# Kernel optimization log

Hardware: AMD Instinct MI355X
Metric: run time of the kernel (lower is better)

## Reference

```python
import jax, jax.numpy as jnp
import numpy as np

START_TAG = 1
END_TAG = 2
NUM_TAGS = 16


def setup_inputs() -> dict:
    key = jax.random.key(0)
    k1, k2, k3 = jax.random.split(key, 3)
    bs, L, T = 4096, 512, NUM_TAGS
    emission = jax.random.normal(k1, (bs, L, T), dtype=jnp.float32)
    tags = jax.random.randint(k2, (bs, L), 0, T, dtype=jnp.int64)
    mask = jnp.ones((bs, L), dtype=jnp.float32)
    # learned transition parameter, initialized as in the torch module
    transition = jax.random.uniform(k3, (T, T), minval=-0.1, maxval=0.1, dtype=jnp.float32)
    transition = transition.at[:, START_TAG].set(-1000.0)
    transition = transition.at[END_TAG, :].set(-1000.0)
    return {"emission": emission, "tags": tags, "mask": mask, "transition": transition}


def _compute_score(emission, tags, mask, transition):
    bs, L, T = emission.shape
    first = tags[:, 0]
    score = transition[START_TAG, first] + jnp.take_along_axis(
        emission[:, 0, :], first[:, None], axis=1).squeeze(1)
    prev_t = tags[:, :-1]
    cur_t = tags[:, 1:]
    trans_s = transition[prev_t, cur_t] * mask[:, 1:]
    em_s = jnp.take_along_axis(emission[:, 1:, :], cur_t[:, :, None], axis=2).squeeze(-1) * mask[:, 1:]
    score = score + (trans_s + em_s).sum(axis=1)
    last_idx = mask.astype(jnp.int32).sum(axis=1) - 1
    last_tags = jnp.take_along_axis(tags, last_idx[:, None].astype(tags.dtype), axis=1).squeeze(1)
    return score + transition[last_tags, END_TAG]


def _compute_dp(emission, mask, transition):
    bs, L, T = emission.shape

    def step(alpha, xs):
        em_t, m_t = xs  # em_t: [bs, T], m_t: [bs]
        # temp[b, prev, cur] = alpha[b, prev] + transition[prev, cur] + em_t[b, cur]
        new = jax.nn.logsumexp(
            alpha[:, :, None] + transition[None, :, :] + em_t[:, None, :], axis=1)
        alpha = m_t[:, None] * new + (1.0 - m_t[:, None]) * alpha
        return alpha, None

    alpha0 = jnp.zeros((bs, T), dtype=emission.dtype)  # faithful: torch.full(.., 0)
    alpha, _ = jax.lax.scan(step, alpha0, (jnp.swapaxes(emission, 0, 1), mask.T))
    alpha = alpha + transition[:, END_TAG][None, :]
    return jax.nn.logsumexp(alpha, axis=1)


def reference(emission, tags, mask, transition):
    score = _compute_score(emission, tags, mask, transition)
    dp = _compute_dp(emission, mask, transition)
    return -jnp.sum(score - dp)
```

## Files before the change

kernel.cpp:

```cpp
#include <hip/hip_runtime.h>

#define BS 4096
#define LL 512
#define NB 16
#define NCH 32
#define HT 256
#define SCWD 130
#define SCW 260
#define START_TAG 1
#define END_TAG 2
#define BIASF 4.5f
#define L2E 1.44269504f
#define LN2 0.69314718055994531f

typedef float f32x4 __attribute__((ext_vector_type(4)));
typedef short s16x4 __attribute__((ext_vector_type(4)));
union BF4 { unsigned u[2]; s16x4 s; };

__device__ __forceinline__ unsigned cvt_pk_bf16(float lo, float hi) {
    unsigned r;
    asm("v_cvt_pk_bf16_f32 %0, %1, %2" : "=v"(r) : "v"(lo), "v"(hi));
    return r;
}
__device__ __forceinline__ float blo(unsigned u) { return __uint_as_float(u << 16); }
__device__ __forceinline__ float bhi(unsigned u) { return __uint_as_float(u & 0xFFFF0000u); }
__device__ __forceinline__ float b2f(unsigned short h) { return __uint_as_float(((unsigned)h) << 16); }

__device__ __forceinline__ void chain16(const unsigned* __restrict__ sSC, int t0l,
                                        int j, int q, const BF4& Af, unsigned mb,
                                        unsigned& p01, unsigned& p23, float& e2f)
{
    const int base = t0l * SCWD + j * 8 + 2 * q;
    uint2 svA = *(const uint2*)(sSC + base);
    if (__all(mb == 0xFFFFu)) {
#pragma unroll
        for (int s = 0; s < 16; ++s) {
            const uint2 svB = (s < 15) ? *(const uint2*)(sSC + base + (s + 1) * SCWD) : svA;
            const float f0 = blo(svA.x), f1 = bhi(svA.x);
            const float f2 = blo(svA.y), f3 = bhi(svA.y);
            BF4 Bf; Bf.u[0] = p01; Bf.u[1] = p23;
            f32x4 z = {0.f, 0.f, 0.f, 0.f};
            f32x4 d = __builtin_amdgcn_mfma_f32_16x16x16bf16_1k(Af.s, Bf.s, z, 0, 0, 0);
            p01 = cvt_pk_bf16(d[0] * f0, d[1] * f1);
            p23 = cvt_pk_bf16(d[2] * f2, d[3] * f3);
            svA = svB;
        }
    } else {
#pragma unroll
        for (int s = 0; s < 16; ++s) {
            const uint2 svB = (s < 15) ? *(const uint2*)(sSC + base + (s + 1) * SCWD) : svA;
            const float f0 = blo(svA.x), f1 = bhi(svA.x);
            const float f2 = blo(svA.y), f3 = bhi(svA.y);
            BF4 Bf; Bf.u[0] = p01; Bf.u[1] = p23;
            f32x4 z = {0.f, 0.f, 0.f, 0.f};
            f32x4 d = __builtin_amdgcn_mfma_f32_16x16x16bf16_1k(Af.s, Bf.s, z, 0, 0, 0);
            const unsigned n01 = cvt_pk_bf16(d[0] * f0, d[1] * f1);
            const unsigned n23 = cvt_pk_bf16(d[2] * f2, d[3] * f3);
            const bool up = ((mb >> s) & 1u) != 0u;
            p01 = up ? n01 : p01;
            p23 = up ? n23 : p23;
            svA = svB;
        }
    }
    const float v0 = blo(p01), v1 = bhi(p01), v2 = blo(p23), v3 = bhi(p23);
    float mm = fmaxf(fmaxf(v0, v1), fmaxf(v2, v3));
    mm = fmaxf(mm, __shfl_xor(mm, 16));
    mm = fmaxf(mm, __shfl_xor(mm, 32));
    if (mm > 0.f) {
        const int ex = (int)((__float_as_uint(mm) >> 23) & 0xFFu) - 127;
        const float sre = __uint_as_float((unsigned)(127 - ex) << 23);
        e2f += (float)ex;
        p01 = cvt_pk_bf16(v0 * sre, v1 * sre);
        p23 = cvt_pk_bf16(v2 * sre, v3 * sre);
    }
}

__global__ __launch_bounds__(1024) void crf_l4(
    const float* __restrict__ em, const int* __restrict__ tg,
    const float* __restrict__ mk, const float* __restrict__ tr,
    float* __restrict__ out)
{
    __shared__ unsigned sSC[HT * SCWD];
    __shared__ unsigned sYp[NCH * NB * 8];
    __shared__ float sYs[NCH][NB], sRs[NCH][NB], sF[NCH][NB], sG[NCH][NB];
    __shared__ unsigned short sMB[NCH][NB];
    __shared__ float sTR[256];
    __shared__ float sSc[NB], sRes[NB];

    const int tid = threadIdx.x;
    const int wv = tid >> 6, lane = tid & 63;
    const int j = lane & 15, q = lane >> 4;
    const long gb0 = (long)blockIdx.x * NB;

    if (tid < 64) *(f32x4*)(sTR + tid * 4) = *(const f32x4*)(tr + tid * 4);

    int is64 = 1;
    {
        const unsigned long long* t64 = (const unsigned long long*)tg;
#pragma unroll
        for (int i = 0; i < 16; ++i) is64 &= (t64[i] < 16ull) ? 1 : 0;
    }
    const int esz = is64 ? 2 : 1;

    {
        const float* mp = mk + (gb0 + wv) * (long)LL;
#pragma unroll
        for (int k = 0; k < 8; ++k) {
            const unsigned long long bal = __ballot(mp[k * 64 + lane] > 0.f);
            if (lane == 0) {
                sMB[4 * k + 0][wv] = (unsigned short)(bal);
                sMB[4 * k + 1][wv] = (unsigned short)(bal >> 16);
                sMB[4 * k + 2][wv] = (unsigned short)(bal >> 32);
                sMB[4 * k + 3][wv] = (unsigned short)(bal >> 48);
            }
        }
    }
    __syncthreads();

    BF4 Af;
    {
        float Ef[4];
#pragma unroll
        for (int i = 0; i < 4; ++i)
            Ef[i] = exp2f(sTR[(q * 4 + i) * 16 + j] * L2E);
        Af.u[0] = cvt_pk_bf16(Ef[0], Ef[1]);
        Af.u[1] = cvt_pk_bf16(Ef[2], Ef[3]);
    }

    float scoreAcc = 0.f;

    for (int h = 0; h < 2; ++h) {
#pragma unroll 4
        for (int it = 0; it < 16; ++it) {
            const int flat = tid * 4 + it * 4096;
            const int bl = flat >> 12, t = (flat >> 4) & 255, r4 = flat & 15;
            const f32x4 v = *(const f32x4*)(em + ((gb0 + bl) * (long)LL + h * HT + t) * 16 + r4);
            const float e0 = exp2f(fmaf(v.x, L2E, -BIASF));
            const float e1 = exp2f(fmaf(v.y, L2E, -BIASF));
            const float e2 = exp2f(fmaf(v.z, L2E, -BIASF));
            const float e3 = exp2f(fmaf(v.w, L2E, -BIASF));
            uint2 w; w.x = cvt_pk_bf16(e0, e1); w.y = cvt_pk_bf16(e2, e3);
            *(uint2*)(sSC + t * SCWD + bl * 8 + (r4 >> 1)) = w;
        }
        __syncthreads();

        {
            const long bb = (gb0 + wv) * (long)LL;
            const unsigned short* sc16 = (const unsigned short*)sSC;
#pragma unroll
            for (int k = 0; k < 4; ++k) {
                const int tl = k * 64 + lane;
                const int t = h * HT + tl;
                const int tcur = tg[(bb + t) * esz];
                const long pidx = (bb + (t == 0 ? 1 : t) - 1) * esz;
                const int tpv = (t == 0) ? START_TAG : tg[pidx];
                const float mbit = (float)((sMB[t >> 4][wv] >> (t & 15)) & 1);
                const float scm = (t == 0) ? 1.f : mbit;
                const float sc = b2f(sc16[tl * SCW + wv * 16 + tcur]);
                const float emr = (log2f(fmaxf(sc, 1e-37f)) + BIASF) * LN2;
                scoreAcc = fmaf(emr + sTR[tpv * 16 + tcur], scm, scoreAcc);
            }
        }

        const int c = h * 16 + wv;
        const unsigned mb = (unsigned)sMB[c][j];
        {
            unsigned p01 = 0x3F803F80u, p23 = 0x3F803F80u;
            float e2f = 0.f;
            chain16(sSC, wv * 16, j, q, Af, mb, p01, p23, e2f);
            uint2 y; y.x = p01; y.y = p23;
            *(uint2*)(sYp + (c * 16 + j) * 8 + 2 * q) = y;
            float sum = blo(p01) + bhi(p01) + blo(p23) + bhi(p23);
            sum += __shfl_xor(sum, 16);
            sum += __shfl_xor(sum, 32);
            if (q == 0) {
                sYs[c][j] = sum;
                sF[c][j] = e2f + BIASF * (float)__popc(mb);
            }
        }
        __syncthreads();

        if (c > 0) {
            const uint2 y = *(const uint2*)(sYp + ((c - 1) * 16 + j) * 8 + 2 * q);
            unsigned p01 = y.x, p23 = y.y;
            float e2f = 0.f;
            chain16(sSC, wv * 16, j, q, Af, mb, p01, p23, e2f);
            float sum = blo(p01) + bhi(p01) + blo(p23) + bhi(p23);
            sum += __shfl_xor(sum, 16);
            sum += __shfl_xor(sum, 32);
            if (q == 0) {
                sRs[c][j] = sum;
                sG[c][j] = e2f + BIASF * (float)__popc(mb);
            }
        }
        __syncthreads();
    }

#pragma unroll
    for (int o = 1; o <= 32; o <<= 1) scoreAcc += __shfl_xor(scoreAcc, o);
    if (lane == 0) sSc[wv] = scoreAcc;
    __syncthreads();

    if (tid < 256) {
        const int b = tid >> 4, row = tid & 15;
        const unsigned short* yp16 = (const unsigned short*)sYp;
        float x = b2f(yp16[((NCH - 1) * 16 + b) * 16 + row])
                * exp2f(sTR[row * 16 + END_TAG] * L2E);
#pragma unroll
        for (int o = 1; o <= 8; o <<= 1) x += __shfl_xor(x, o, 16);
        if (row == 0) {
            float l2 = log2f(fmaxf(x, 1e-37f)) + sF[0][b];
#pragma unroll
            for (int c2 = 1; c2 < NCH; ++c2)
                l2 += log2f(fmaxf(sRs[c2][b], 1e-37f))
                    - log2f(fmaxf(sYs[c2][b], 1e-37f)) + sG[c2][b];
            int cnt = 0;
#pragma unroll
            for (int c2 = 0; c2 < NCH; ++c2) cnt += __popc((unsigned)sMB[c2][b]);
            const int li = (cnt > 0) ? (cnt - 1) : 0;
            const int lt = tg[((gb0 + b) * (long)LL + li) * esz];
            sRes[b] = LN2 * l2 - (sSc[b] + sTR[lt * 16 + END_TAG]);
        }
    }
    __syncthreads();
    if (tid == 0) {
        float s = 0.f;
#pragma unroll
        for (int i = 0; i < NB; ++i) s += sRes[i];
        atomicAdd(out, s);
    }
}

extern "C" void kernel_launch(void* const* d_in, const int* in_sizes, int n_in,
                              void* d_out, int out_size, void* d_ws, size_t ws_size,
                              hipStream_t stream) {
    const float* em = (const float*)d_in[0];
    const int*   tg = (const int*)d_in[1];
    const float* mk = (const float*)d_in[2];
    const float* tr = (const float*)d_in[3];
    float* out = (float*)d_out;

    hipMemsetAsync(out, 0, sizeof(float), stream);
    crf_l4<<<BS / NB, 1024, 0, stream>>>(em, tg, mk, tr, out);
}
```

Baseline: 52.52 us.

## Halve batches per block and interleave two independent chunk chains per wave

Blocks now hold 8 sequences with 512 threads instead of 16 with 1024, which doubles the grid. Each wave now advances two independent 16-step time chunks at once (chunks c and c+8), so their dependent MFMA and convert sequences can interleave and hide each other's latency. The price is that only 8 of the 16 MFMA columns carry distinct sequences, since the upper 8 lanes duplicate the lower ones, and each wave holds more registers. Shared-memory strides and indexing are resized to match.

```diff
diff --git a/kernel.cpp b/kernel.cpp
--- a/kernel.cpp
+++ b/kernel.cpp
@@ -2,11 +2,11 @@
 
 #define BS 4096
 #define LL 512
-#define NB 16
+#define NB 8
 #define NCH 32
 #define HT 256
-#define SCWD 130
-#define SCW 260
+#define SCWD 65
+#define SCW 130
 #define START_TAG 1
 #define END_TAG 2
 #define BIASF 4.5f
@@ -26,56 +26,73 @@
 __device__ __forceinline__ float bhi(unsigned u) { return __uint_as_float(u & 0xFFFF0000u); }
 __device__ __forceinline__ float b2f(unsigned short h) { return __uint_as_float(((unsigned)h) << 16); }
 
-__device__ __forceinline__ void chain16(const unsigned* __restrict__ sSC, int t0l,
-                                        int j, int q, const BF4& Af, unsigned mb,
-                                        unsigned& p01, unsigned& p23, float& e2f)
+#define CSTEP(SV, P01, P23) { \
+        const float f0 = blo((SV).x), f1 = bhi((SV).x); \
+        const float f2 = blo((SV).y), f3 = bhi((SV).y); \
+        BF4 Bf; Bf.u[0] = P01; Bf.u[1] = P23; \
+        f32x4 z = {0.f, 0.f, 0.f, 0.f}; \
+        f32x4 d = __builtin_amdgcn_mfma_f32_16x16x16bf16_1k(Af.s, Bf.s, z, 0, 0, 0); \
+        P01 = cvt_pk_bf16(d[0] * f0, d[1] * f1); \
+        P23 = cvt_pk_bf16(d[2] * f2, d[3] * f3); }
+
+#define CSTEPM(SV, MB, S, P01, P23) { \
+        const float f0 = blo((SV).x), f1 = bhi((SV).x); \
+        const float f2 = blo((SV).y), f3 = bhi((SV).y); \
+        BF4 Bf; Bf.u[0] = P01; Bf.u[1] = P23; \
+        f32x4 z = {0.f, 0.f, 0.f, 0.f}; \
+        f32x4 d = __builtin_amdgcn_mfma_f32_16x16x16bf16_1k(Af.s, Bf.s, z, 0, 0, 0); \
+        const unsigned n01 = cvt_pk_bf16(d[0] * f0, d[1] * f1); \
+        const unsigned n23 = cvt_pk_bf16(d[2] * f2, d[3] * f3); \
+        const bool up = (((MB) >> (S)) & 1u) != 0u; \
+        P01 = up ? n01 : P01; \
+        P23 = up ? n23 : P23; }
+
+#define RENORM(P01, P23, E2F) { \
+        const float v0 = blo(P01), v1 = bhi(P01), v2 = blo(P23), v3 = bhi(P23); \
+        float mm = fmaxf(fmaxf(v0, v1), fmaxf(v2, v3)); \
+        mm = fmaxf(mm, __shfl_xor(mm, 16)); \
+        mm = fmaxf(mm, __shfl_xor(mm, 32)); \
+        if (mm > 0.f) { \
+            const int ex = (int)((__float_as_uint(mm) >> 23) & 0xFFu) - 127; \
+            const float sre = __uint_as_float((unsigned)(127 - ex) << 23); \
+            E2F += (float)ex; \
+            P01 = cvt_pk_bf16(v0 * sre, v1 * sre); \
+            P23 = cvt_pk_bf16(v2 * sre, v3 * sre); } }
+
+__device__ __forceinline__ void chain16_dual(
+    const unsigned* __restrict__ sSC, int ta, int tb, int jq_off, const BF4& Af,
+    unsigned mba, unsigned mbb,
+    unsigned& a01, unsigned& a23, unsigned& b01, unsigned& b23,
+    float& ea, float& eb)
 {
-    const int base = t0l * SCWD + j * 8 + 2 * q;
-    uint2 svA = *(const uint2*)(sSC + base);
-    if (__all(mb == 0xFFFFu)) {
+    const int basea = ta * SCWD + jq_off;
+    const int baseb = tb * SCWD + jq_off;
+    uint2 svA = *(const uint2*)(sSC + basea);
+    uint2 svB = *(const uint2*)(sSC + baseb);
+    if (__all((mba == 0xFFFFu) & (mbb == 0xFFFFu))) {
 #pragma unroll
         for (int s = 0; s < 16; ++s) {
-            const uint2 svB = (s < 15) ? *(const uint2*)(sSC + base + (s + 1) * SCWD) : svA;
-            const float f0 = blo(svA.x), f1 = bhi(svA.x);
-            const float f2 = blo(svA.y), f3 = bhi(svA.y);
-            BF4 Bf; Bf.u[0] = p01; Bf.u[1] = p23;
-            f32x4 z = {0.f, 0.f, 0.f, 0.f};
-            f32x4 d = __builtin_amdgcn_mfma_f32_16x16x16bf16_1k(Af.s, Bf.s, z, 0, 0, 0);
-            p01 = cvt_pk_bf16(d[0] * f0, d[1] * f1);
-            p23 = cvt_pk_bf16(d[2] * f2, d[3] * f3);
-            svA = svB;
+            const uint2 nA = (s < 15) ? *(const uint2*)(sSC + basea + (s + 1) * SCWD) : svA;
+            const uint2 nB = (s < 15) ? *(const uint2*)(sSC + baseb + (s + 1) * SCWD) : svB;
+            CSTEP(svA, a01, a23)
+            CSTEP(svB, b01, b23)
+            svA = nA; svB = nB;
         }
     } else {
 #pragma unroll
         for (int s = 0; s < 16; ++s) {
-            const uint2 svB = (s < 15) ? *(const uint2*)(sSC + base + (s + 1) * SCWD) : svA;
-            const float f0 = blo(svA.x), f1 = bhi(svA.x);
-            const float f2 = blo(svA.y), f3 = bhi(svA.y);
-            BF4 Bf; Bf.u[0] = p01; Bf.u[1] = p23;
-            f32x4 z = {0.f, 0.f, 0.f, 0.f};
-            f32x4 d = __builtin_amdgcn_mfma_f32_16x16x16bf16_1k(Af.s, Bf.s, z, 0, 0, 0);
-            const unsigned n01 = cvt_pk_bf16(d[0] * f0, d[1] * f1);
-            const unsigned n23 = cvt_pk_bf16(d[2] * f2, d[3] * f3);
-            const bool up = ((mb >> s) & 1u) != 0u;
-            p01 = up ? n01 : p01;
-            p23 = up ? n23 : p23;
-            svA = svB;
-        }
-    }
-    const float v0 = blo(p01), v1 = bhi(p01), v2 = blo(p23), v3 = bhi(p23);
-    float mm = fmaxf(fmaxf(v0, v1), fmaxf(v2, v3));
-    mm = fmaxf(mm, __shfl_xor(mm, 16));
-    mm = fmaxf(mm, __shfl_xor(mm, 32));
-    if (mm > 0.f) {
-        const int ex = (int)((__float_as_uint(mm) >> 23) & 0xFFu) - 127;
-        const float sre = __uint_as_float((unsigned)(127 - ex) << 23);
-        e2f += (float)ex;
-        p01 = cvt_pk_bf16(v0 * sre, v1 * sre);
-        p23 = cvt_pk_bf16(v2 * sre, v3 * sre);
-    }
-}
-
-__global__ __launch_bounds__(1024) void crf_l4(
+            const uint2 nA = (s < 15) ? *(const uint2*)(sSC + basea + (s + 1) * SCWD) : svA;
+            const uint2 nB = (s < 15) ? *(const uint2*)(sSC + baseb + (s + 1) * SCWD) : svB;
+            CSTEPM(svA, mba, s, a01, a23)
+            CSTEPM(svB, mbb, s, b01, b23)
+            svA = nA; svB = nB;
+        }
+    }
+    RENORM(a01, a23, ea)
+    RENORM(b01, b23, eb)
+}
+
+__global__ __launch_bounds__(512) void crf_p2(
     const float* __restrict__ em, const int* __restrict__ tg,
     const float* __restrict__ mk, const float* __restrict__ tr,
     float* __restrict__ out)
@@ -90,6 +107,7 @@
     const int tid = threadIdx.x;
     const int wv = tid >> 6, lane = tid & 63;
     const int j = lane & 15, q = lane >> 4;
+    const int jj = j & 7;
     const long gb0 = (long)blockIdx.x * NB;
 
     if (tid < 64) *(f32x4*)(sTR + tid * 4) = *(const f32x4*)(tr + tid * 4);
@@ -126,13 +144,14 @@
         Af.u[0] = cvt_pk_bf16(Ef[0], Ef[1]);
         Af.u[1] = cvt_pk_bf16(Ef[2], Ef[3]);
     }
+    const int jq_off = jj * 8 + 2 * q;
 
     float scoreAcc = 0.f;
 
     for (int h = 0; h < 2; ++h) {
 #pragma unroll 4
         for (int it = 0; it < 16; ++it) {
-            const int flat = tid * 4 + it * 4096;
+            const int flat = tid * 4 + it * 2048;
             const int bl = flat >> 12, t = (flat >> 4) & 255, r4 = flat & 15;
             const f32x4 v = *(const f32x4*)(em + ((gb0 + bl) * (long)LL + h * HT + t) * 16 + r4);
             const float e0 = exp2f(fmaf(v.x, L2E, -BIASF));
@@ -162,35 +181,45 @@
             }
         }
 
-        const int c = h * 16 + wv;
-        const unsigned mb = (unsigned)sMB[c][j];
+        const int c1 = h * 16 + wv, c2 = c1 + 8;
+        const unsigned mb1 = (unsigned)sMB[c1][jj];
+        const unsigned mb2 = (unsigned)sMB[c2][jj];
         {
-            unsigned p01 = 0x3F803F80u, p23 = 0x3F803F80u;
-            float e2f = 0.f;
-            chain16(sSC, wv * 16, j, q, Af, mb, p01, p23, e2f);
-            uint2 y; y.x = p01; y.y = p23;
-            *(uint2*)(sYp + (c * 16 + j) * 8 + 2 * q) = y;
-            float sum = blo(p01) + bhi(p01) + blo(p23) + bhi(p23);
-            sum += __shfl_xor(sum, 16);
-            sum += __shfl_xor(sum, 32);
-            if (q == 0) {
-                sYs[c][j] = sum;
-                sF[c][j] = e2f + BIASF * (float)__popc(mb);
+            unsigned a01 = 0x3F803F80u, a23 = 0x3F803F80u;
+            unsigned b01 = 0x3F803F80u, b23 = 0x3F803F80u;
+            float ea = 0.f, eb = 0.f;
+            chain16_dual(sSC, wv * 16, (wv + 8) * 16, jq_off, Af,
+                         mb1, mb2, a01, a23, b01, b23, ea, eb);
+            uint2 ya; ya.x = a01; ya.y = a23;
+            uint2 yb; yb.x = b01; yb.y = b23;
+            *(uint2*)(sYp + (c1 * NB + jj) * 8 + 2 * q) = ya;
+            *(uint2*)(sYp + (c2 * NB + jj) * 8 + 2 * q) = yb;
+            float sa = blo(a01) + bhi(a01) + blo(a23) + bhi(a23);
+            float sb = blo(b01) + bhi(b01) + blo(b23) + bhi(b23);
+            sa += __shfl_xor(sa, 16); sa += __shfl_xor(sa, 32);
+            sb += __shfl_xor(sb, 16); sb += __shfl_xor(sb, 32);
+            if (lane < 8) {
+                sYs[c1][jj] = sa; sF[c1][jj] = ea + BIASF * (float)__popc(mb1);
+                sYs[c2][jj] = sb; sF[c2][jj] = eb + BIASF * (float)__popc(mb2);
             }
         }
         __syncthreads();
 
-        if (c > 0) {
-            const uint2 y = *(const uint2*)(sYp + ((c - 1) * 16 + j) * 8 + 2 * q);
-            unsigned p01 = y.x, p23 = y.y;
-            float e2f = 0.f;
-            chain16(sSC, wv * 16, j, q, Af, mb, p01, p23, e2f);
-            float sum = blo(p01) + bhi(p01) + blo(p23) + bhi(p23);
-            sum += __shfl_xor(sum, 16);
-            sum += __shfl_xor(sum, 32);
-            if (q == 0) {
-                sRs[c][j] = sum;
-                sG[c][j] = e2f + BIASF * (float)__popc(mb);
+        {
+            const int p1 = (c1 > 0) ? (c1 - 1) : 0;
+            const uint2 y1 = *(const uint2*)(sYp + (p1 * NB + jj) * 8 + 2 * q);
+            const uint2 y2 = *(const uint2*)(sYp + ((c2 - 1) * NB + jj) * 8 + 2 * q);
+            unsigned a01 = y1.x, a23 = y1.y, b01 = y2.x, b23 = y2.y;
+            float ea = 0.f, eb = 0.f;
+            chain16_dual(sSC, wv * 16, (wv + 8) * 16, jq_off, Af,
+                         mb1, mb2, a01, a23, b01, b23, ea, eb);
+            float sa = blo(a01) + bhi(a01) + blo(a23) + bhi(a23);
+            float sb = blo(b01) + bhi(b01) + blo(b23) + bhi(b23);
+            sa += __shfl_xor(sa, 16); sa += __shfl_xor(sa, 32);
+            sb += __shfl_xor(sb, 16); sb += __shfl_xor(sb, 32);
+            if (lane < 8) {
+                sRs[c1][jj] = sa; sG[c1][jj] = ea + BIASF * (float)__popc(mb1);
+                sRs[c2][jj] = sb; sG[c2][jj] = eb + BIASF * (float)__popc(mb2);
             }
         }
         __syncthreads();
@@ -201,22 +230,22 @@
     if (lane == 0) sSc[wv] = scoreAcc;
     __syncthreads();
 
-    if (tid < 256) {
+    if (tid < 128) {
         const int b = tid >> 4, row = tid & 15;
         const unsigned short* yp16 = (const unsigned short*)sYp;
-        float x = b2f(yp16[((NCH - 1) * 16 + b) * 16 + row])
+        float x = b2f(yp16[((NCH - 1) * NB + b) * 16 + row])
                 * exp2f(sTR[row * 16 + END_TAG] * L2E);
 #pragma unroll
         for (int o = 1; o <= 8; o <<= 1) x += __shfl_xor(x, o, 16);
         if (row == 0) {
             float l2 = log2f(fmaxf(x, 1e-37f)) + sF[0][b];
 #pragma unroll
-            for (int c2 = 1; c2 < NCH; ++c2)
-                l2 += log2f(fmaxf(sRs[c2][b], 1e-37f))
-                    - log2f(fmaxf(sYs[c2][b], 1e-37f)) + sG[c2][b];
+            for (int c = 1; c < NCH; ++c)
+                l2 += log2f(fmaxf(sRs[c][b], 1e-37f))
+                    - log2f(fmaxf(sYs[c][b], 1e-37f)) + sG[c][b];
             int cnt = 0;
 #pragma unroll
-            for (int c2 = 0; c2 < NCH; ++c2) cnt += __popc((unsigned)sMB[c2][b]);
+            for (int c = 0; c < NCH; ++c) cnt += __popc((unsigned)sMB[c][b]);
             const int li = (cnt > 0) ? (cnt - 1) : 0;
             const int lt = tg[((gb0 + b) * (long)LL + li) * esz];
             sRes[b] = LN2 * l2 - (sSc[b] + sTR[lt * 16 + END_TAG]);
@@ -241,5 +270,5 @@
     float* out = (float*)d_out;
 
     hipMemsetAsync(out, 0, sizeof(float), stream);
-    crf_l4<<<BS / NB, 1024, 0, stream>>>(em, tg, mk, tr, out);
-}
+    crf_p2<<<BS / NB, 512, 0, stream>>>(em, tg, mk, tr, out);
+}
```

Result: slower. 80.31 us (+52.9%).
